# Performance work log

Hardware: AMD Instinct MI355X
Metric: run time of the kernel (lower is better)

## Reference

```python
import jax, jax.numpy as jnp
import numpy as np

B, S, D, H = 4, 512, 768, 200


def setup_inputs() -> dict:
    key = jax.random.key(0)
    ks = jax.random.split(key, 6)
    x = jax.random.normal(ks[0], (B, S, D), dtype=jnp.float32)
    # Linear default init ~ U(-1/sqrt(fan_in), 1/sqrt(fan_in)); scaled normal is fine for a baseline
    W_head = jax.random.normal(ks[1], (D, H), dtype=jnp.float32) * (1.0 / np.sqrt(D))
    b_head = jnp.zeros((H,), dtype=jnp.float32)
    W_tail = jax.random.normal(ks[2], (D, H), dtype=jnp.float32) * (1.0 / np.sqrt(D))
    b_tail = jnp.zeros((H,), dtype=jnp.float32)
    # xavier_normal on [200,200,200]: fan_in = fan_out = 200*200 -> std = sqrt(2/80000)
    U = jax.random.normal(ks[3], (H, H, H), dtype=jnp.float32) * np.sqrt(2.0 / (2 * H * H))
    W_down = jax.random.normal(ks[4], (H, 1), dtype=jnp.float32) * (1.0 / np.sqrt(H))
    b_down = jnp.zeros((1,), dtype=jnp.float32)
    return {"x": x, "W_head": W_head, "b_head": b_head, "W_tail": W_tail,
            "b_tail": b_tail, "U": U, "W_down": W_down, "b_down": b_down}


def reference(x, W_head, b_head, W_tail, b_tail, U, W_down, b_down):
    # head/tail projections with ReLU: [B,S,H]
    head = jax.nn.relu(x @ W_head + b_head)
    tail = jax.nn.relu(x @ W_tail + b_tail)
    # biaffine: 'bxi,oij,byj->bxyo' done as two contractions
    tmp = jnp.einsum('bxi,oij->bxoj', head, U)            # [B,S,H,H]
    logits = jnp.einsum('bxoj,byj->bxyo', tmp, tail)       # [B,S,S,H] (== permuted boxy)
    # down_layer(200->1).squeeze(-1); rope branch in source is dead (rope_logits = 0)
    scores = (logits @ W_down)[..., 0] + b_down[0]         # [B,S,S]
    return scores / jnp.sqrt(jnp.asarray(200.0, dtype=scores.dtype))
```

## Files before the change

### kernel.cpp

```cpp
#include <hip/hip_runtime.h>

#define H 200
#define D 768
#define BATCH 4
#define S 512
#define M (BATCH*S)
#define KP 224
#define NP 208
#define NCAT 400
#define OG 8

typedef __attribute__((ext_vector_type(8))) short bf16x8;
typedef __attribute__((ext_vector_type(4))) float f32x4;
typedef unsigned short us;

__device__ inline us f2bf(float f) {
    union { float f; unsigned u; } v; v.f = f;
    return (us)((v.u + 0x7FFF + ((v.u >> 16) & 1)) >> 16);
}

__global__ void cvt_x(const float4* __restrict__ x4, ushort4* __restrict__ xb4) {
    int t = blockIdx.x * 256 + threadIdx.x;
    float4 v = x4[t];
    ushort4 o; o.x = f2bf(v.x); o.y = f2bf(v.y); o.z = f2bf(v.z); o.w = f2bf(v.w);
    xb4[t] = o;
}

__global__ void cvt_W(const float* __restrict__ Wh, const float* __restrict__ Wt,
                      us* __restrict__ Wcb) {
    int id = blockIdx.x * 256 + threadIdx.x;
    if (id >= NCAT * D) return;
    int n = id / D, k = id % D;
    float v = (n < H) ? Wh[k * H + n] : Wt[k * H + (n - H)];
    Wcb[id] = f2bf(v);
}

__global__ void reduceU_part(const float4* __restrict__ U4, const float* __restrict__ Wd,
                             float4* __restrict__ P4) {
    int t = blockIdx.x * 256 + threadIdx.x;
    if (t >= H * H / 4) return;
    int g = blockIdx.y;
    float4 acc = make_float4(0.f, 0.f, 0.f, 0.f);
    int o0 = g * (H / OG);
    #pragma unroll 5
    for (int o = o0; o < o0 + H / OG; ++o) {
        float w = Wd[o];
        float4 u = U4[o * (H * H / 4) + t];
        acc.x += w * u.x; acc.y += w * u.y; acc.z += w * u.z; acc.w += w * u.w;
    }
    P4[g * (H * H / 4) + t] = acc;
}

__global__ void cvt_V(const float* __restrict__ P, us* __restrict__ VTb) {
    int id = blockIdx.x * 256 + threadIdx.x;
    if (id >= NP * KP) return;
    int n = id / KP, k = id % KP;
    float s = 0.f;
    if (n < H && k < H) {
        #pragma unroll
        for (int g = 0; g < OG; ++g) s += P[g * H * H + k * H + n];
    }
    VTb[id] = f2bf(s);
}

__global__ __launch_bounds__(64) void proj_mfma(
        const us* __restrict__ xb, const us* __restrict__ Wcb,
        const float* __restrict__ bh, const float* __restrict__ bt,
        us* __restrict__ headb, us* __restrict__ tailb) {
    int lane = threadIdx.x, quad = lane >> 4, col = lane & 15;
    int m0 = blockIdx.x * 32, n0 = blockIdx.y * 16;
    const bf16x8* A0 = (const bf16x8*)(xb + (m0 + col) * D + quad * 8);
    const bf16x8* A1 = (const bf16x8*)(xb + (m0 + 16 + col) * D + quad * 8);
    const bf16x8* Bp = (const bf16x8*)(Wcb + (n0 + col) * D + quad * 8);
    f32x4 acc0 = {0.f,0.f,0.f,0.f}, acc1 = {0.f,0.f,0.f,0.f};
    #pragma unroll 4
    for (int kk = 0; kk < D / 32; ++kk) {
        bf16x8 a0 = A0[kk * 4];
        bf16x8 a1 = A1[kk * 4];
        bf16x8 b  = Bp[kk * 4];
        acc0 = __builtin_amdgcn_mfma_f32_16x16x32_bf16(a0, b, acc0, 0, 0, 0);
        acc1 = __builtin_amdgcn_mfma_f32_16x16x32_bf16(a1, b, acc1, 0, 0, 0);
    }
    int n = n0 + col;
    float bias; us* dst; int nn;
    if (n < H) { bias = bh[n];     dst = headb; nn = n; }
    else       { bias = bt[n - H]; dst = tailb; nn = n - H; }
    #pragma unroll
    for (int r = 0; r < 4; ++r) {
        int ma = m0 + quad * 4 + r;
        dst[ma * KP + nn]        = f2bf(fmaxf(acc0[r] + bias, 0.f));
        dst[(ma + 16) * KP + nn] = f2bf(fmaxf(acc1[r] + bias, 0.f));
    }
}

__global__ __launch_bounds__(64) void hv_mfma(
        const us* __restrict__ headb, const us* __restrict__ VTb,
        us* __restrict__ hvb) {
    int lane = threadIdx.x, quad = lane >> 4, col = lane & 15;
    int m0 = blockIdx.x * 32, n0 = blockIdx.y * 16;
    const bf16x8* A0 = (const bf16x8*)(headb + (m0 + col) * KP + quad * 8);
    const bf16x8* A1 = (const bf16x8*)(headb + (m0 + 16 + col) * KP + quad * 8);
    const bf16x8* Bp = (const bf16x8*)(VTb + (n0 + col) * KP + quad * 8);
    f32x4 acc0 = {0.f,0.f,0.f,0.f}, acc1 = {0.f,0.f,0.f,0.f};
    #pragma unroll
    for (int kk = 0; kk < KP / 32; ++kk) {
        bf16x8 a0 = A0[kk * 4];
        bf16x8 a1 = A1[kk * 4];
        bf16x8 b  = Bp[kk * 4];
        acc0 = __builtin_amdgcn_mfma_f32_16x16x32_bf16(a0, b, acc0, 0, 0, 0);
        acc1 = __builtin_amdgcn_mfma_f32_16x16x32_bf16(a1, b, acc1, 0, 0, 0);
    }
    int n = n0 + col;
    #pragma unroll
    for (int r = 0; r < 4; ++r) {
        int ma = m0 + quad * 4 + r;
        hvb[ma * KP + n]        = f2bf(acc0[r]);
        hvb[(ma + 16) * KP + n] = f2bf(acc1[r]);
    }
}

__global__ __launch_bounds__(64) void scores_mfma(
        const us* __restrict__ hvb, const us* __restrict__ tailb,
        const float* __restrict__ bd, float* __restrict__ out) {
    int lane = threadIdx.x, quad = lane >> 4, col = lane & 15;
    int b = blockIdx.z;
    int m0 = blockIdx.x * 32, n0 = blockIdx.y * 32;
    const us* A  = hvb   + b * S * KP;
    const us* Bm = tailb + b * S * KP;
    const bf16x8* A0 = (const bf16x8*)(A  + (m0 + col) * KP + quad * 8);
    const bf16x8* A1 = (const bf16x8*)(A  + (m0 + 16 + col) * KP + quad * 8);
    const bf16x8* B0 = (const bf16x8*)(Bm + (n0 + col) * KP + quad * 8);
    const bf16x8* B1 = (const bf16x8*)(Bm + (n0 + 16 + col) * KP + quad * 8);
    f32x4 a00 = {0.f,0.f,0.f,0.f}, a01 = {0.f,0.f,0.f,0.f};
    f32x4 a10 = {0.f,0.f,0.f,0.f}, a11 = {0.f,0.f,0.f,0.f};
    #pragma unroll
    for (int kk = 0; kk < KP / 32; ++kk) {
        bf16x8 a0 = A0[kk * 4];
        bf16x8 a1 = A1[kk * 4];
        bf16x8 b0 = B0[kk * 4];
        bf16x8 b1 = B1[kk * 4];
        a00 = __builtin_amdgcn_mfma_f32_16x16x32_bf16(a0, b0, a00, 0, 0, 0);
        a01 = __builtin_amdgcn_mfma_f32_16x16x32_bf16(a0, b1, a01, 0, 0, 0);
        a10 = __builtin_amdgcn_mfma_f32_16x16x32_bf16(a1, b0, a10, 0, 0, 0);
        a11 = __builtin_amdgcn_mfma_f32_16x16x32_bf16(a1, b1, a11, 0, 0, 0);
    }
    float bias = bd[0];
    const float scale = 0.07071067811865475f;
    float* outb = out + b * S * S;
    #pragma unroll
    for (int r = 0; r < 4; ++r) {
        int ma = m0 + quad * 4 + r, mb = ma + 16;
        outb[ma * S + n0 + col]      = (a00[r] + bias) * scale;
        outb[ma * S + n0 + 16 + col] = (a01[r] + bias) * scale;
        outb[mb * S + n0 + col]      = (a10[r] + bias) * scale;
        outb[mb * S + n0 + 16 + col] = (a11[r] + bias) * scale;
    }
}

extern "C" void kernel_launch(void* const* d_in, const int* in_sizes, int n_in,
                              void* d_out, int out_size, void* d_ws, size_t ws_size,
                              hipStream_t stream) {
    const float* x  = (const float*)d_in[0];
    const float* Wh = (const float*)d_in[1];
    const float* bh = (const float*)d_in[2];
    const float* Wt = (const float*)d_in[3];
    const float* bt = (const float*)d_in[4];
    const float* U  = (const float*)d_in[5];
    const float* Wd = (const float*)d_in[6];
    const float* bd = (const float*)d_in[7];
    float* out = (float*)d_out;

    us* xb    = (us*)d_ws;
    us* Wcb   = xb  + (size_t)M * D;
    us* VTb   = Wcb + (size_t)NCAT * D;
    us* hvb   = VTb + (size_t)NP * KP;
    us* headb = hvb + (size_t)M * KP;
    us* tailb = headb + (size_t)M * KP;
    float* P  = (float*)headb;

    cvt_x<<<(M * D / 4) / 256, 256, 0, stream>>>((const float4*)x, (ushort4*)xb);
    cvt_W<<<(NCAT * D + 255) / 256, 256, 0, stream>>>(Wh, Wt, Wcb);
    reduceU_part<<<dim3((H * H / 4 + 255) / 256, OG), 256, 0, stream>>>(
        (const float4*)U, Wd, (float4*)P);
    cvt_V<<<(NP * KP + 255) / 256, 256, 0, stream>>>(P, VTb);
    hipMemsetAsync(headb, 0, (size_t)2 * M * KP * sizeof(us), stream);
    hipMemsetAsync(hvb, 0, (size_t)M * KP * sizeof(us), stream);
    proj_mfma<<<dim3(M / 32, NCAT / 16), 64, 0, stream>>>(xb, Wcb, bh, bt, headb, tailb);
    hv_mfma<<<dim3(M / 32, NP / 16), 64, 0, stream>>>(headb, VTb, hvb);
    scores_mfma<<<dim3(S / 32, S / 32, BATCH), 64, 0, stream>>>(hvb, tailb, bd, out);
}
```

Before: 130.2 us.

## Fuse all stages into one cooperative persistent kernel with grid syncs

Replaces seven kernel launches and two memsets with a single cooperative kernel of 512 blocks. Stages are separated by grid.sync(), and only the padding columns are zeroed instead of whole buffers. The scores stage now uses one 32x16 tile per wave instead of 32x32, matching a fixed grid of 2048 waves. This removes launch and memset overhead, but adds grid-wide barrier cost and less per-wave reuse in the scores GEMM.

```diff
diff --git a/kernel.cpp b/kernel.cpp
--- a/kernel.cpp
+++ b/kernel.cpp
@@ -1,4 +1,7 @@
 #include <hip/hip_runtime.h>
+#include <hip/hip_cooperative_groups.h>
+
+namespace cg = cooperative_groups;
 
 #define H 200
 #define D 768
@@ -9,6 +12,8 @@
 #define NP 208
 #define NCAT 400
 #define OG 8
+#define GBLK 512
+#define NTHREADS 256
 
 typedef __attribute__((ext_vector_type(8))) short bf16x8;
 typedef __attribute__((ext_vector_type(4))) float f32x4;
@@ -19,173 +24,172 @@
     return (us)((v.u + 0x7FFF + ((v.u >> 16) & 1)) >> 16);
 }
 
-__global__ void cvt_x(const float4* __restrict__ x4, ushort4* __restrict__ xb4) {
-    int t = blockIdx.x * 256 + threadIdx.x;
-    float4 v = x4[t];
-    ushort4 o; o.x = f2bf(v.x); o.y = f2bf(v.y); o.z = f2bf(v.z); o.w = f2bf(v.w);
-    xb4[t] = o;
-}
+__global__ __launch_bounds__(NTHREADS) void mega(
+        const float* __restrict__ x,  const float* __restrict__ Wh,
+        const float* __restrict__ bh, const float* __restrict__ Wt,
+        const float* __restrict__ bt, const float* __restrict__ U,
+        const float* __restrict__ Wd, const float* __restrict__ bd,
+        float* __restrict__ out, unsigned char* __restrict__ ws) {
+    cg::grid_group grid = cg::this_grid();
 
-__global__ void cvt_W(const float* __restrict__ Wh, const float* __restrict__ Wt,
-                      us* __restrict__ Wcb) {
-    int id = blockIdx.x * 256 + threadIdx.x;
-    if (id >= NCAT * D) return;
-    int n = id / D, k = id % D;
-    float v = (n < H) ? Wh[k * H + n] : Wt[k * H + (n - H)];
-    Wcb[id] = f2bf(v);
-}
+    us* xb    = (us*)ws;
+    us* Wcb   = xb    + (size_t)M * D;
+    us* VTb   = Wcb   + (size_t)NCAT * D;
+    us* hvb   = VTb   + (size_t)NP * KP;
+    us* headb = hvb   + (size_t)M * KP;
+    us* tailb = headb + (size_t)M * KP;
+    float* P  = (float*)(tailb + (size_t)M * KP);
 
-__global__ void reduceU_part(const float4* __restrict__ U4, const float* __restrict__ Wd,
-                             float4* __restrict__ P4) {
-    int t = blockIdx.x * 256 + threadIdx.x;
-    if (t >= H * H / 4) return;
-    int g = blockIdx.y;
-    float4 acc = make_float4(0.f, 0.f, 0.f, 0.f);
-    int o0 = g * (H / OG);
-    #pragma unroll 5
-    for (int o = o0; o < o0 + H / OG; ++o) {
-        float w = Wd[o];
-        float4 u = U4[o * (H * H / 4) + t];
-        acc.x += w * u.x; acc.y += w * u.y; acc.z += w * u.z; acc.w += w * u.w;
+    const int gtid = blockIdx.x * NTHREADS + threadIdx.x;
+    const int GTH  = GBLK * NTHREADS;
+    const int wid  = gtid >> 6;
+    const int lane = threadIdx.x & 63;
+    const int quad = lane >> 4, col = lane & 15;
+
+    {
+        const float4* x4 = (const float4*)x;
+        ushort4* xb4 = (ushort4*)xb;
+        for (int t = gtid; t < M * D / 4; t += GTH) {
+            float4 v = x4[t];
+            ushort4 o; o.x = f2bf(v.x); o.y = f2bf(v.y); o.z = f2bf(v.z); o.w = f2bf(v.w);
+            xb4[t] = o;
+        }
+        for (int id = gtid; id < NCAT * D; id += GTH) {
+            int n = id / D, k = id % D;
+            float v = (n < H) ? Wh[k * H + n] : Wt[k * H + (n - H)];
+            Wcb[id] = f2bf(v);
+        }
+        const float4* U4 = (const float4*)U;
+        float4* P4 = (float4*)P;
+        for (int task = gtid; task < OG * (H * H / 4); task += GTH) {
+            int g = task / (H * H / 4), t = task % (H * H / 4);
+            float4 acc = make_float4(0.f, 0.f, 0.f, 0.f);
+            int o0 = g * (H / OG);
+            #pragma unroll 5
+            for (int o = o0; o < o0 + H / OG; ++o) {
+                float w = Wd[o];
+                float4 u = U4[o * (H * H / 4) + t];
+                acc.x += w * u.x; acc.y += w * u.y; acc.z += w * u.z; acc.w += w * u.w;
+            }
+            P4[g * (H * H / 4) + t] = acc;
+        }
     }
-    P4[g * (H * H / 4) + t] = acc;
-}
+    grid.sync();
 
-__global__ void cvt_V(const float* __restrict__ P, us* __restrict__ VTb) {
-    int id = blockIdx.x * 256 + threadIdx.x;
-    if (id >= NP * KP) return;
-    int n = id / KP, k = id % KP;
-    float s = 0.f;
-    if (n < H && k < H) {
+    {
+        for (int id = gtid; id < M * (KP - H); id += GTH) {
+            int r = id / (KP - H), c = H + id % (KP - H);
+            headb[r * KP + c] = 0; tailb[r * KP + c] = 0;
+        }
+        for (int id = gtid; id < M * (KP - NP); id += GTH) {
+            int r = id / (KP - NP), c = NP + id % (KP - NP);
+            hvb[r * KP + c] = 0;
+        }
+        for (int id = gtid; id < NP * KP; id += GTH) {
+            int n = id / KP, k = id % KP;
+            float s = 0.f;
+            if (n < H && k < H) {
+                #pragma unroll
+                for (int g = 0; g < OG; ++g) s += P[g * H * H + k * H + n];
+            }
+            VTb[id] = f2bf(s);
+        }
+        if (wid < (M / 32) * (NCAT / 16)) {
+            int m0 = (wid % (M / 32)) * 32, n0 = (wid / (M / 32)) * 16;
+            const bf16x8* A0 = (const bf16x8*)(xb + (m0 + col) * D + quad * 8);
+            const bf16x8* A1 = (const bf16x8*)(xb + (m0 + 16 + col) * D + quad * 8);
+            const bf16x8* Bp = (const bf16x8*)(Wcb + (n0 + col) * D + quad * 8);
+            f32x4 acc0 = {0.f,0.f,0.f,0.f}, acc1 = {0.f,0.f,0.f,0.f};
+            #pragma unroll 4
+            for (int kk = 0; kk < D / 32; ++kk) {
+                bf16x8 a0 = A0[kk * 4];
+                bf16x8 a1 = A1[kk * 4];
+                bf16x8 b  = Bp[kk * 4];
+                acc0 = __builtin_amdgcn_mfma_f32_16x16x32_bf16(a0, b, acc0, 0, 0, 0);
+                acc1 = __builtin_amdgcn_mfma_f32_16x16x32_bf16(a1, b, acc1, 0, 0, 0);
+            }
+            int n = n0 + col;
+            float bias; us* dst; int nn;
+            if (n < H) { bias = bh[n];     dst = headb; nn = n; }
+            else       { bias = bt[n - H]; dst = tailb; nn = n - H; }
+            #pragma unroll
+            for (int r = 0; r < 4; ++r) {
+                int ma = m0 + quad * 4 + r;
+                dst[ma * KP + nn]        = f2bf(fmaxf(acc0[r] + bias, 0.f));
+                dst[(ma + 16) * KP + nn] = f2bf(fmaxf(acc1[r] + bias, 0.f));
+            }
+        }
+    }
+    grid.sync();
+
+    if (wid < (M / 32) * (NP / 16)) {
+        int m0 = (wid % (M / 32)) * 32, n0 = (wid / (M / 32)) * 16;
+        const bf16x8* A0 = (const bf16x8*)(headb + (m0 + col) * KP + quad * 8);
+        const bf16x8* A1 = (const bf16x8*)(headb + (m0 + 16 + col) * KP + quad * 8);
+        const bf16x8* Bp = (const bf16x8*)(VTb + (n0 + col) * KP + quad * 8);
+        f32x4 acc0 = {0.f,0.f,0.f,0.f}, acc1 = {0.f,0.f,0.f,0.f};
         #pragma unroll
-        for (int g = 0; g < OG; ++g) s += P[g * H * H + k * H + n];
+        for (int kk = 0; kk < KP / 32; ++kk) {
+            bf16x8 a0 = A0[kk * 4];
+            bf16x8 a1 = A1[kk * 4];
+            bf16x8 b  = Bp[kk * 4];
+            acc0 = __builtin_amdgcn_mfma_f32_16x16x32_bf16(a0, b, acc0, 0, 0, 0);
+            acc1 = __builtin_amdgcn_mfma_f32_16x16x32_bf16(a1, b, acc1, 0, 0, 0);
+        }
+        int n = n0 + col;
+        #pragma unroll
+        for (int r = 0; r < 4; ++r) {
+            int ma = m0 + quad * 4 + r;
+            hvb[ma * KP + n]        = f2bf(acc0[r]);
+            hvb[(ma + 16) * KP + n] = f2bf(acc1[r]);
+        }
     }
-    VTb[id] = f2bf(s);
-}
+    grid.sync();
 
-__global__ __launch_bounds__(64) void proj_mfma(
-        const us* __restrict__ xb, const us* __restrict__ Wcb,
-        const float* __restrict__ bh, const float* __restrict__ bt,
-        us* __restrict__ headb, us* __restrict__ tailb) {
-    int lane = threadIdx.x, quad = lane >> 4, col = lane & 15;
-    int m0 = blockIdx.x * 32, n0 = blockIdx.y * 16;
-    const bf16x8* A0 = (const bf16x8*)(xb + (m0 + col) * D + quad * 8);
-    const bf16x8* A1 = (const bf16x8*)(xb + (m0 + 16 + col) * D + quad * 8);
-    const bf16x8* Bp = (const bf16x8*)(Wcb + (n0 + col) * D + quad * 8);
-    f32x4 acc0 = {0.f,0.f,0.f,0.f}, acc1 = {0.f,0.f,0.f,0.f};
-    #pragma unroll 4
-    for (int kk = 0; kk < D / 32; ++kk) {
-        bf16x8 a0 = A0[kk * 4];
-        bf16x8 a1 = A1[kk * 4];
-        bf16x8 b  = Bp[kk * 4];
-        acc0 = __builtin_amdgcn_mfma_f32_16x16x32_bf16(a0, b, acc0, 0, 0, 0);
-        acc1 = __builtin_amdgcn_mfma_f32_16x16x32_bf16(a1, b, acc1, 0, 0, 0);
-    }
-    int n = n0 + col;
-    float bias; us* dst; int nn;
-    if (n < H) { bias = bh[n];     dst = headb; nn = n; }
-    else       { bias = bt[n - H]; dst = tailb; nn = n - H; }
-    #pragma unroll
-    for (int r = 0; r < 4; ++r) {
-        int ma = m0 + quad * 4 + r;
-        dst[ma * KP + nn]        = f2bf(fmaxf(acc0[r] + bias, 0.f));
-        dst[(ma + 16) * KP + nn] = f2bf(fmaxf(acc1[r] + bias, 0.f));
-    }
-}
-
-__global__ __launch_bounds__(64) void hv_mfma(
-        const us* __restrict__ headb, const us* __restrict__ VTb,
-        us* __restrict__ hvb) {
-    int lane = threadIdx.x, quad = lane >> 4, col = lane & 15;
-    int m0 = blockIdx.x * 32, n0 = blockIdx.y * 16;
-    const bf16x8* A0 = (const bf16x8*)(headb + (m0 + col) * KP + quad * 8);
-    const bf16x8* A1 = (const bf16x8*)(headb + (m0 + 16 + col) * KP + quad * 8);
-    const bf16x8* Bp = (const bf16x8*)(VTb + (n0 + col) * KP + quad * 8);
-    f32x4 acc0 = {0.f,0.f,0.f,0.f}, acc1 = {0.f,0.f,0.f,0.f};
-    #pragma unroll
-    for (int kk = 0; kk < KP / 32; ++kk) {
-        bf16x8 a0 = A0[kk * 4];
-        bf16x8 a1 = A1[kk * 4];
-        bf16x8 b  = Bp[kk * 4];
-        acc0 = __builtin_amdgcn_mfma_f32_16x16x32_bf16(a0, b, acc0, 0, 0, 0);
-        acc1 = __builtin_amdgcn_mfma_f32_16x16x32_bf16(a1, b, acc1, 0, 0, 0);
-    }
-    int n = n0 + col;
-    #pragma unroll
-    for (int r = 0; r < 4; ++r) {
-        int ma = m0 + quad * 4 + r;
-        hvb[ma * KP + n]        = f2bf(acc0[r]);
-        hvb[(ma + 16) * KP + n] = f2bf(acc1[r]);
-    }
-}
-
-__global__ __launch_bounds__(64) void scores_mfma(
-        const us* __restrict__ hvb, const us* __restrict__ tailb,
-        const float* __restrict__ bd, float* __restrict__ out) {
-    int lane = threadIdx.x, quad = lane >> 4, col = lane & 15;
-    int b = blockIdx.z;
-    int m0 = blockIdx.x * 32, n0 = blockIdx.y * 32;
-    const us* A  = hvb   + b * S * KP;
-    const us* Bm = tailb + b * S * KP;
-    const bf16x8* A0 = (const bf16x8*)(A  + (m0 + col) * KP + quad * 8);
-    const bf16x8* A1 = (const bf16x8*)(A  + (m0 + 16 + col) * KP + quad * 8);
-    const bf16x8* B0 = (const bf16x8*)(Bm + (n0 + col) * KP + quad * 8);
-    const bf16x8* B1 = (const bf16x8*)(Bm + (n0 + 16 + col) * KP + quad * 8);
-    f32x4 a00 = {0.f,0.f,0.f,0.f}, a01 = {0.f,0.f,0.f,0.f};
-    f32x4 a10 = {0.f,0.f,0.f,0.f}, a11 = {0.f,0.f,0.f,0.f};
-    #pragma unroll
-    for (int kk = 0; kk < KP / 32; ++kk) {
-        bf16x8 a0 = A0[kk * 4];
-        bf16x8 a1 = A1[kk * 4];
-        bf16x8 b0 = B0[kk * 4];
-        bf16x8 b1 = B1[kk * 4];
-        a00 = __builtin_amdgcn_mfma_f32_16x16x32_bf16(a0, b0, a00, 0, 0, 0);
-        a01 = __builtin_amdgcn_mfma_f32_16x16x32_bf16(a0, b1, a01, 0, 0, 0);
-        a10 = __builtin_amdgcn_mfma_f32_16x16x32_bf16(a1, b0, a10, 0, 0, 0);
-        a11 = __builtin_amdgcn_mfma_f32_16x16x32_bf16(a1, b1, a11, 0, 0, 0);
-    }
-    float bias = bd[0];
-    const float scale = 0.07071067811865475f;
-    float* outb = out + b * S * S;
-    #pragma unroll
-    for (int r = 0; r < 4; ++r) {
-        int ma = m0 + quad * 4 + r, mb = ma + 16;
-        outb[ma * S + n0 + col]      = (a00[r] + bias) * scale;
-        outb[ma * S + n0 + 16 + col] = (a01[r] + bias) * scale;
-        outb[mb * S + n0 + col]      = (a10[r] + bias) * scale;
-        outb[mb * S + n0 + 16 + col] = (a11[r] + bias) * scale;
+    {
+        int b  = wid >> 9;
+        int r9 = wid & 511;
+        int m0 = (r9 & 15) * 32, n0 = (r9 >> 4) * 16;
+        const us* A  = hvb   + (size_t)b * S * KP;
+        const us* Bm = tailb + (size_t)b * S * KP;
+        const bf16x8* A0 = (const bf16x8*)(A  + (m0 + col) * KP + quad * 8);
+        const bf16x8* A1 = (const bf16x8*)(A  + (m0 + 16 + col) * KP + quad * 8);
+        const bf16x8* Bp = (const bf16x8*)(Bm + (n0 + col) * KP + quad * 8);
+        f32x4 acc0 = {0.f,0.f,0.f,0.f}, acc1 = {0.f,0.f,0.f,0.f};
+        #pragma unroll
+        for (int kk = 0; kk < KP / 32; ++kk) {
+            bf16x8 a0 = A0[kk * 4];
+            bf16x8 a1 = A1[kk * 4];
+            bf16x8 b8 = Bp[kk * 4];
+            acc0 = __builtin_amdgcn_mfma_f32_16x16x32_bf16(a0, b8, acc0, 0, 0, 0);
+            acc1 = __builtin_amdgcn_mfma_f32_16x16x32_bf16(a1, b8, acc1, 0, 0, 0);
+        }
+        float bias = bd[0];
+        const float scale = 0.07071067811865475f;
+        float* outb = out + (size_t)b * S * S;
+        #pragma unroll
+        for (int r = 0; r < 4; ++r) {
+            int ma = m0 + quad * 4 + r;
+            outb[ma * S + n0 + col]        = (acc0[r] + bias) * scale;
+            outb[(ma + 16) * S + n0 + col] = (acc1[r] + bias) * scale;
+        }
     }
 }
 
 extern "C" void kernel_launch(void* const* d_in, const int* in_sizes, int n_in,
                               void* d_out, int out_size, void* d_ws, size_t ws_size,
                               hipStream_t stream) {
-    const float* x  = (const float*)d_in[0];
-    const float* Wh = (const float*)d_in[1];
-    const float* bh = (const float*)d_in[2];
-    const float* Wt = (const float*)d_in[3];
-    const float* bt = (const float*)d_in[4];
-    const float* U  = (const float*)d_in[5];
-    const float* Wd = (const float*)d_in[6];
-    const float* bd = (const float*)d_in[7];
-    float* out = (float*)d_out;
-
-    us* xb    = (us*)d_ws;
-    us* Wcb   = xb  + (size_t)M * D;
-    us* VTb   = Wcb + (size_t)NCAT * D;
-    us* hvb   = VTb + (size_t)NP * KP;
-    us* headb = hvb + (size_t)M * KP;
-    us* tailb = headb + (size_t)M * KP;
-    float* P  = (float*)headb;
-
-    cvt_x<<<(M * D / 4) / 256, 256, 0, stream>>>((const float4*)x, (ushort4*)xb);
-    cvt_W<<<(NCAT * D + 255) / 256, 256, 0, stream>>>(Wh, Wt, Wcb);
-    reduceU_part<<<dim3((H * H / 4 + 255) / 256, OG), 256, 0, stream>>>(
-        (const float4*)U, Wd, (float4*)P);
-    cvt_V<<<(NP * KP + 255) / 256, 256, 0, stream>>>(P, VTb);
-    hipMemsetAsync(headb, 0, (size_t)2 * M * KP * sizeof(us), stream);
-    hipMemsetAsync(hvb, 0, (size_t)M * KP * sizeof(us), stream);
-    proj_mfma<<<dim3(M / 32, NCAT / 16), 64, 0, stream>>>(xb, Wcb, bh, bt, headb, tailb);
-    hv_mfma<<<dim3(M / 32, NP / 16), 64, 0, stream>>>(headb, VTb, hvb);
-    scores_mfma<<<dim3(S / 32, S / 32, BATCH), 64, 0, stream>>>(hvb, tailb, bd, out);
+    const void* x  = d_in[0];
+    const void* Wh = d_in[1];
+    const void* bh = d_in[2];
+    const void* Wt = d_in[3];
+    const void* bt = d_in[4];
+    const void* U  = d_in[5];
+    const void* Wd = d_in[6];
+    const void* bd = d_in[7];
+    void* outp = d_out;
+    void* wsp  = d_ws;
+    void* args[] = { &x, &Wh, &bh, &Wt, &bt, &U, &Wd, &bd, &outp, &wsp };
+    hipLaunchCooperativeKernel((void*)mega, dim3(GBLK), dim3(NTHREADS),
+                               args, 0, stream);
 }
```

Result: slower. 333.4 us (+156.1%).

## Fuse preprocessing kernels and memsets into one prep kernel

Applied to the files above, without the earlier changes.

Replaces four preprocessing kernels and two memsets with a single prep kernel. Some blocks reduce U against W_down, combining two halves through shared memory and writing the transposed bf16 V directly, which drops the intermediate partial buffer and the separate cvt_V pass. The remaining blocks convert x and W with grid-stride loops and zero only the padding columns instead of memsetting whole buffers. This cuts launch count and memory traffic, but the U reduction now runs on only 79 blocks, which may leave less parallelism on that path.

```diff
diff --git a/kernel.cpp b/kernel.cpp
--- a/kernel.cpp
+++ b/kernel.cpp
@@ -8,7 +8,8 @@
 #define KP 224
 #define NP 208
 #define NCAT 400
-#define OG 8
+#define VT_BLOCKS 79
+#define PREP_BLOCKS 1000
 
 typedef __attribute__((ext_vector_type(8))) short bf16x8;
 typedef __attribute__((ext_vector_type(4))) float f32x4;
@@ -19,48 +20,74 @@
     return (us)((v.u + 0x7FFF + ((v.u >> 16) & 1)) >> 16);
 }
 
-__global__ void cvt_x(const float4* __restrict__ x4, ushort4* __restrict__ xb4) {
-    int t = blockIdx.x * 256 + threadIdx.x;
-    float4 v = x4[t];
-    ushort4 o; o.x = f2bf(v.x); o.y = f2bf(v.y); o.z = f2bf(v.z); o.w = f2bf(v.w);
-    xb4[t] = o;
-}
-
-__global__ void cvt_W(const float* __restrict__ Wh, const float* __restrict__ Wt,
-                      us* __restrict__ Wcb) {
-    int id = blockIdx.x * 256 + threadIdx.x;
-    if (id >= NCAT * D) return;
-    int n = id / D, k = id % D;
-    float v = (n < H) ? Wh[k * H + n] : Wt[k * H + (n - H)];
-    Wcb[id] = f2bf(v);
-}
-
-__global__ void reduceU_part(const float4* __restrict__ U4, const float* __restrict__ Wd,
-                             float4* __restrict__ P4) {
-    int t = blockIdx.x * 256 + threadIdx.x;
-    if (t >= H * H / 4) return;
-    int g = blockIdx.y;
-    float4 acc = make_float4(0.f, 0.f, 0.f, 0.f);
-    int o0 = g * (H / OG);
-    #pragma unroll 5
-    for (int o = o0; o < o0 + H / OG; ++o) {
-        float w = Wd[o];
-        float4 u = U4[o * (H * H / 4) + t];
-        acc.x += w * u.x; acc.y += w * u.y; acc.z += w * u.z; acc.w += w * u.w;
-    }
-    P4[g * (H * H / 4) + t] = acc;
-}
-
-__global__ void cvt_V(const float* __restrict__ P, us* __restrict__ VTb) {
-    int id = blockIdx.x * 256 + threadIdx.x;
-    if (id >= NP * KP) return;
-    int n = id / KP, k = id % KP;
-    float s = 0.f;
-    if (n < H && k < H) {
-        #pragma unroll
-        for (int g = 0; g < OG; ++g) s += P[g * H * H + k * H + n];
-    }
-    VTb[id] = f2bf(s);
+__global__ __launch_bounds__(256) void prep(
+        const float* __restrict__ x,  const float* __restrict__ Wh,
+        const float* __restrict__ Wt, const float* __restrict__ U,
+        const float* __restrict__ Wd,
+        us* __restrict__ xb, us* __restrict__ Wcb, us* __restrict__ VTb,
+        us* __restrict__ headb, us* __restrict__ tailb, us* __restrict__ hvb) {
+    int bid = blockIdx.x;
+    if (bid < VT_BLOCKS) {
+        __shared__ float4 red[128];
+        int c = threadIdx.x & 127, half = threadIdx.x >> 7;
+        int t = bid * 128 + c;
+        const float4* U4 = (const float4*)U;
+        float4 acc = make_float4(0.f, 0.f, 0.f, 0.f);
+        if (t < H * H / 4) {
+            int o0 = half * (H / 2);
+            #pragma unroll 10
+            for (int o = o0; o < o0 + H / 2; ++o) {
+                float w = Wd[o];
+                float4 u = U4[o * (H * H / 4) + t];
+                acc.x += w * u.x; acc.y += w * u.y;
+                acc.z += w * u.z; acc.w += w * u.w;
+            }
+        }
+        if (half == 1) red[c] = acc;
+        __syncthreads();
+        if (half == 0 && t < H * H / 4) {
+            float4 r = red[c];
+            acc.x += r.x; acc.y += r.y; acc.z += r.z; acc.w += r.w;
+            int i = t / (H / 4), j0 = (t % (H / 4)) * 4;
+            VTb[(j0 + 0) * KP + i] = f2bf(acc.x);
+            VTb[(j0 + 1) * KP + i] = f2bf(acc.y);
+            VTb[(j0 + 2) * KP + i] = f2bf(acc.z);
+            VTb[(j0 + 3) * KP + i] = f2bf(acc.w);
+        }
+        return;
+    }
+    const int GTH = (PREP_BLOCKS - VT_BLOCKS) * 256;
+    int gtid = (bid - VT_BLOCKS) * 256 + threadIdx.x;
+    {
+        const float4* x4 = (const float4*)x;
+        ushort4* xb4 = (ushort4*)xb;
+        for (int t = gtid; t < M * D / 4; t += GTH) {
+            float4 v = x4[t];
+            ushort4 o; o.x = f2bf(v.x); o.y = f2bf(v.y); o.z = f2bf(v.z); o.w = f2bf(v.w);
+            xb4[t] = o;
+        }
+    }
+    for (int id = gtid; id < NCAT * D; id += GTH) {
+        int n = id / D, k = id % D;
+        float v = (n < H) ? Wh[k * H + n] : Wt[k * H + (n - H)];
+        Wcb[id] = f2bf(v);
+    }
+    for (int id = gtid; id < M * (KP - H); id += GTH) {
+        int r = id / (KP - H), c = H + id % (KP - H);
+        headb[r * KP + c] = 0; tailb[r * KP + c] = 0;
+    }
+    for (int id = gtid; id < M * (KP - NP); id += GTH) {
+        int r = id / (KP - NP), c = NP + id % (KP - NP);
+        hvb[r * KP + c] = 0;
+    }
+    for (int id = gtid; id < H * (KP - H); id += GTH) {
+        int n = id / (KP - H), k = H + id % (KP - H);
+        VTb[n * KP + k] = 0;
+    }
+    for (int id = gtid; id < (NP - H) * KP; id += GTH) {
+        int n = H + id / KP, k = id % KP;
+        VTb[n * KP + k] = 0;
+    }
 }
 
 __global__ __launch_bounds__(64) void proj_mfma(
@@ -125,8 +152,8 @@
     int lane = threadIdx.x, quad = lane >> 4, col = lane & 15;
     int b = blockIdx.z;
     int m0 = blockIdx.x * 32, n0 = blockIdx.y * 32;
-    const us* A  = hvb   + b * S * KP;
-    const us* Bm = tailb + b * S * KP;
+    const us* A  = hvb   + (size_t)b * S * KP;
+    const us* Bm = tailb + (size_t)b * S * KP;
     const bf16x8* A0 = (const bf16x8*)(A  + (m0 + col) * KP + quad * 8);
     const bf16x8* A1 = (const bf16x8*)(A  + (m0 + 16 + col) * KP + quad * 8);
     const bf16x8* B0 = (const bf16x8*)(Bm + (n0 + col) * KP + quad * 8);
@@ -146,7 +173,7 @@
     }
     float bias = bd[0];
     const float scale = 0.07071067811865475f;
-    float* outb = out + b * S * S;
+    float* outb = out + (size_t)b * S * S;
     #pragma unroll
     for (int r = 0; r < 4; ++r) {
         int ma = m0 + quad * 4 + r, mb = ma + 16;
@@ -171,20 +198,14 @@
     float* out = (float*)d_out;
 
     us* xb    = (us*)d_ws;
-    us* Wcb   = xb  + (size_t)M * D;
-    us* VTb   = Wcb + (size_t)NCAT * D;
-    us* hvb   = VTb + (size_t)NP * KP;
-    us* headb = hvb + (size_t)M * KP;
+    us* Wcb   = xb    + (size_t)M * D;
+    us* VTb   = Wcb   + (size_t)NCAT * D;
+    us* hvb   = VTb   + (size_t)NP * KP;
+    us* headb = hvb   + (size_t)M * KP;
     us* tailb = headb + (size_t)M * KP;
-    float* P  = (float*)headb;
-
-    cvt_x<<<(M * D / 4) / 256, 256, 0, stream>>>((const float4*)x, (ushort4*)xb);
-    cvt_W<<<(NCAT * D + 255) / 256, 256, 0, stream>>>(Wh, Wt, Wcb);
-    reduceU_part<<<dim3((H * H / 4 + 255) / 256, OG), 256, 0, stream>>>(
-        (const float4*)U, Wd, (float4*)P);
-    cvt_V<<<(NP * KP + 255) / 256, 256, 0, stream>>>(P, VTb);
-    hipMemsetAsync(headb, 0, (size_t)2 * M * KP * sizeof(us), stream);
-    hipMemsetAsync(hvb, 0, (size_t)M * KP * sizeof(us), stream);
+
+    prep<<<PREP_BLOCKS, 256, 0, stream>>>(x, Wh, Wt, U, Wd,
+                                          xb, Wcb, VTb, headb, tailb, hvb);
     proj_mfma<<<dim3(M / 32, NCAT / 16), 64, 0, stream>>>(xb, Wcb, bh, bt, headb, tailb);
     hv_mfma<<<dim3(M / 32, NP / 16), 64, 0, stream>>>(headb, VTb, hvb);
     scores_mfma<<<dim3(S / 32, S / 32, BATCH), 64, 0, stream>>>(hvb, tailb, bd, out);
```

After: 119.7 us. 1.09x faster.
